# Kernel optimization log

Hardware: AMD Instinct MI355X
Metric: run time of the kernel (lower is better)

Reference implementation:

```python
import jax, jax.numpy as jnp
import numpy as np

B = 131072      # batch
G = 8           # number of groups
GS = 8          # features per group (n_features = G*GS = 64)
K = 8           # n_basis
O = 16          # kan_out_dim
TOT = G * O     # 128, GroupKANLayer output dim
R = 10          # n_rules
FIN = 20        # fuzzy_in_dim = max(2*n_rules, 8)
EPS_BN = 1e-5


def setup_inputs() -> dict:
    key = jax.random.key(0)
    ks = jax.random.split(key, 8)
    x = jax.random.normal(ks[0], (B, G * GS), dtype=jnp.float32)
    # per-group GaussianRBF params (one shared RBF per group, applied to each feature)
    rbf_centres = jnp.tile(jnp.linspace(-3.0, 3.0, K, dtype=jnp.float32)[None, :], (G, 1))
    rbf_log_widths = jnp.zeros((G, K), dtype=jnp.float32)
    rbf_weights = jax.random.normal(ks[1], (G, K), dtype=jnp.float32) * 0.1
    rbf_linear_w = jnp.ones((G,), dtype=jnp.float32)
    # group projections: kaiming normal fan_in (relu gain sqrt(2))
    proj_W = jax.random.normal(ks[2], (G, O, GS), dtype=jnp.float32) * np.sqrt(2.0 / GS)
    proj_b = jnp.zeros((G, O), dtype=jnp.float32)
    bn1_gamma = jnp.ones((TOT,), dtype=jnp.float32)
    bn1_beta = jnp.zeros((TOT,), dtype=jnp.float32)
    # fuzzy_proj linear (xavier uniform) TOT -> FIN
    a = np.sqrt(6.0 / (TOT + FIN))
    fp_W = jax.random.uniform(ks[3], (FIN, TOT), dtype=jnp.float32, minval=-a, maxval=a)
    fp_b = jnp.zeros((FIN,), dtype=jnp.float32)
    bn2_gamma = jnp.ones((FIN,), dtype=jnp.float32)
    bn2_beta = jnp.zeros((FIN,), dtype=jnp.float32)
    # IT2 fuzzy layer params
    fz_centres = jax.random.uniform(ks[4], (R, FIN), dtype=jnp.float32, minval=-1.0, maxval=1.0)
    fz_log_su = jnp.full((R, FIN), -0.7, dtype=jnp.float32)
    fz_log_sl = jnp.full((R, FIN), -1.2, dtype=jnp.float32)
    # sparse rule head
    head_W = jax.random.normal(ks[5], (1, R), dtype=jnp.float32) * 0.05
    head_b = jnp.zeros((1,), dtype=jnp.float32)
    return {
        'x': x, 'rbf_centres': rbf_centres, 'rbf_log_widths': rbf_log_widths,
        'rbf_weights': rbf_weights, 'rbf_linear_w': rbf_linear_w,
        'proj_W': proj_W, 'proj_b': proj_b,
        'bn1_gamma': bn1_gamma, 'bn1_beta': bn1_beta,
        'fp_W': fp_W, 'fp_b': fp_b, 'bn2_gamma': bn2_gamma, 'bn2_beta': bn2_beta,
        'fz_centres': fz_centres, 'fz_log_su': fz_log_su, 'fz_log_sl': fz_log_sl,
        'head_W': head_W, 'head_b': head_b,
    }


def _batchnorm(h, gamma, beta):
    # training-mode BatchNorm1d: normalize with batch mean / biased variance
    mu = h.mean(axis=0)
    var = h.var(axis=0)
    return (h - mu) * jax.lax.rsqrt(var + EPS_BN) * gamma + beta


def _forward(x, rbf_centres, rbf_log_widths, rbf_weights, rbf_linear_w,
             proj_W, proj_b, bn1_gamma, bn1_beta, fp_W, fp_b,
             bn2_gamma, bn2_beta, fz_centres, fz_log_su, fz_log_sl,
             head_W, head_b):
    b = x.shape[0]
    xg = x.reshape(b, G, GS)                               # groups are contiguous index slices
    sigma = jnp.exp(rbf_log_widths) + 1e-6                 # [G,K]
    # Gaussian RBF over all groups/features at once: [B,G,GS,K]
    rbf = jnp.exp(-0.5 * ((xg[..., None] - rbf_centres[:, None, :]) / sigma[:, None, :]) ** 2)
    act = rbf_linear_w[None, :, None] * xg + jnp.einsum('bgfk,gk->bgf', rbf, rbf_weights)
    proj = jnp.einsum('bgf,gof->bgo', act, proj_W) + proj_b  # grouped linear, [B,G,O]
    h = _batchnorm(proj.reshape(b, TOT), bn1_gamma, bn1_beta)
    # fuzzy_proj: Linear -> BN -> GELU (torch default GELU = exact erf form)
    z = _batchnorm(h @ fp_W.T + fp_b, bn2_gamma, bn2_beta)
    z = jax.nn.gelu(z, approximate=False)                    # [B,FIN]
    # IT2 fuzzy memberships
    su = jnp.exp(fz_log_su) + 1e-6                           # [R,FIN]
    sl = jnp.minimum(jnp.exp(fz_log_sl) + 1e-6, su * 0.9)
    diff = z[:, None, :] - fz_centres[None]                  # [B,R,FIN]
    upper = jnp.exp(-0.5 * (diff / su[None]) ** 2).mean(-1)  # [B,R]
    lower = jnp.exp(-0.5 * (diff / sl[None]) ** 2).mean(-1)
    firing = 0.5 * (upper + lower)
    return firing @ head_W.T + head_b                        # [B,1]


def reference(x, rbf_centres, rbf_log_widths, rbf_weights, rbf_linear_w,
              proj_W, proj_b, bn1_gamma, bn1_beta, fp_W, fp_b,
              bn2_gamma, bn2_beta, fz_centres, fz_log_su, fz_log_sl,
              head_W, head_b):
    return _forward(x, rbf_centres, rbf_log_widths, rbf_weights, rbf_linear_w,
                    proj_W, proj_b, bn1_gamma, bn1_beta, fp_W, fp_b,
                    bn2_gamma, bn2_beta, fz_centres, fz_log_su, fz_log_sl,
                    head_W, head_b)
```

## Files before the change

### kernel.cpp

```cpp
#include <hip/hip_runtime.h>
#include <hip/hip_fp16.h>
#include <math.h>

#define B_N 131072

#define WS_STAT1 0
#define ST1_SZ   (64 * 352)
#define WS_MT    22528
#define WS_C     23808
#define WS_STAT2 23840
#define WS_NH    26400
#define WS_ACTH  26816
#define WS_Z     (26816 + (size_t)B_N * 32)
#define WS_END   (WS_Z + (size_t)B_N * 20)

struct alignas(16) H8 { __half2 a, b, c, d; };

__device__ __forceinline__ float gelu_exact(float v) {
    return 0.5f * v * (1.0f + erff(v * 0.70710678118654752440f));
}

__global__ __launch_bounds__(256) void k_act_moments(
    const float* __restrict__ x, const float* __restrict__ cen,
    const float* __restrict__ lw, const float* __restrict__ rw,
    const float* __restrict__ linw, __half* __restrict__ act_h,
    float* __restrict__ stat1, int store)
{
    __shared__ float sAcc[4][8][44];
    const int t = threadIdx.x;
    const int g = t & 7;
    const int rl = t >> 3;

    float c_[8], nh_[8], w_[8];
#pragma unroll
    for (int k = 0; k < 8; ++k) {
        c_[k] = cen[g * 8 + k];
        float s = expf(lw[g * 8 + k]) + 1e-6f;
        nh_[k] = -0.5f / (s * s);
        w_[k] = rw[g * 8 + k];
    }
    const float lin = linw[g];
    const float c0 = c_[0], nh0 = nh_[0];
    const float delta = c_[1] - c_[0];

    bool uni = true;
#pragma unroll
    for (int k = 0; k < 8; ++k) {
        float ck = c0 + (float)k * delta;
        uni = uni && (fabsf(c_[k] - ck) <= 1e-5f * (1.0f + fabsf(ck)));
        uni = uni && (fabsf(nh_[k] - nh0) <= 1e-6f * fabsf(nh0));
    }
    const bool fast = (bool)__all((int)uni);

    float W_[8];
    float k1 = 0.0f;
    if (fast) {
        k1 = -2.0f * delta * nh0;
#pragma unroll
        for (int k = 0; k < 8; ++k) {
            float kd = (float)k * delta;
            W_[k] = w_[k] * __expf(nh0 * kd * kd);
        }
    }

    float sumA[8], P[36];
#pragma unroll
    for (int f = 0; f < 8; ++f) sumA[f] = 0.0f;
#pragma unroll
    for (int i = 0; i < 36; ++i) P[i] = 0.0f;

    if (fast) {
#pragma unroll 1
        for (int row = blockIdx.x * 32 + rl; row < B_N; row += gridDim.x * 32) {
            const float* xr = x + (size_t)row * 64 + g * 8;
            float4 v0 = *(const float4*)(xr);
            float4 v1 = *(const float4*)(xr + 4);
            float xv[8] = {v0.x, v0.y, v0.z, v0.w, v1.x, v1.y, v1.z, v1.w};
            float act[8];
#pragma unroll
            for (int f = 0; f < 8; ++f) {
                float v = xv[f];
                float dv = v - c0;
                float E0 = __expf(nh0 * dv * dv);
                float T  = __expf(k1 * dv);
                float poly = W_[7];
#pragma unroll
                for (int k = 6; k >= 0; --k) poly = poly * T + W_[k];
                act[f] = lin * v + E0 * poly;
            }
            if (store) {
                H8 h;
                h.a = __floats2half2_rn(act[0], act[1]);
                h.b = __floats2half2_rn(act[2], act[3]);
                h.c = __floats2half2_rn(act[4], act[5]);
                h.d = __floats2half2_rn(act[6], act[7]);
                *(H8*)(act_h + (size_t)row * 64 + g * 8) = h;
            }
            int idx = 0;
#pragma unroll
            for (int f = 0; f < 8; ++f) {
                sumA[f] += act[f];
#pragma unroll
                for (int f2 = 0; f2 <= f; ++f2) { P[idx] += act[f] * act[f2]; ++idx; }
            }
        }
    } else {
#pragma unroll 1
        for (int row = blockIdx.x * 32 + rl; row < B_N; row += gridDim.x * 32) {
            const float* xr = x + (size_t)row * 64 + g * 8;
            float4 v0 = *(const float4*)(xr);
            float4 v1 = *(const float4*)(xr + 4);
            float xv[8] = {v0.x, v0.y, v0.z, v0.w, v1.x, v1.y, v1.z, v1.w};
            float act[8];
#pragma unroll
            for (int f = 0; f < 8; ++f) {
                float v = xv[f];
                float a = lin * v;
#pragma unroll
                for (int k = 0; k < 8; ++k) {
                    float d = v - c_[k];
                    a += w_[k] * __expf(d * d * nh_[k]);
                }
                act[f] = a;
            }
            if (store) {
                H8 h;
                h.a = __floats2half2_rn(act[0], act[1]);
                h.b = __floats2half2_rn(act[2], act[3]);
                h.c = __floats2half2_rn(act[4], act[5]);
                h.d = __floats2half2_rn(act[6], act[7]);
                *(H8*)(act_h + (size_t)row * 64 + g * 8) = h;
            }
            int idx = 0;
#pragma unroll
            for (int f = 0; f < 8; ++f) {
                sumA[f] += act[f];
#pragma unroll
                for (int f2 = 0; f2 <= f; ++f2) { P[idx] += act[f] * act[f2]; ++idx; }
            }
        }
    }

#pragma unroll
    for (int off = 32; off >= 8; off >>= 1) {
#pragma unroll
        for (int f = 0; f < 8; ++f) sumA[f] += __shfl_down(sumA[f], off, 64);
#pragma unroll
        for (int i = 0; i < 36; ++i) P[i] += __shfl_down(P[i], off, 64);
    }
    const int wave = t >> 6, lane = t & 63;
    if (lane < 8) {
        float* dst = &sAcc[wave][lane][0];
#pragma unroll
        for (int f = 0; f < 8; ++f) dst[f] = sumA[f];
#pragma unroll
        for (int i = 0; i < 36; ++i) dst[8 + i] = P[i];
    }
    __syncthreads();
    for (int i = t; i < 352; i += 256) {
        int gg = i / 44, v = i % 44;
        float s = sAcc[0][gg][v] + sAcc[1][gg][v] + sAcc[2][gg][v] + sAcc[3][gg][v];
        atomicAdd(&stat1[(blockIdx.x & 63) * 352 + i], s);
    }
}

__global__ __launch_bounds__(256) void k_build(
    const float* __restrict__ stat1, const float* __restrict__ fpW,
    const float* __restrict__ fpb, const float* __restrict__ g1,
    const float* __restrict__ b1, const float* __restrict__ Wp,
    const float* __restrict__ pb, const float* __restrict__ lsu,
    const float* __restrict__ lsl,
    float* __restrict__ Mt, float* __restrict__ Cc, float* __restrict__ nh,
    float* __restrict__ stat2)
{
    __shared__ float Am[8][8];
    __shared__ float Sg[8][36];
    __shared__ float a_[128], bb_[128];
    const int t = threadIdx.x;
    for (int i = t; i < 352; i += 256) {
        float s = 0.0f;
        for (int st = 0; st < 64; ++st) s += stat1[st * 352 + i];
        float m = s * (1.0f / B_N);
        int g = i / 44, v = i % 44;
        if (v < 8) Am[g][v] = m; else Sg[g][v - 8] = m;
    }
    __syncthreads();
    if (t < 128) {
        const int g = t >> 4;
        float wv[8];
#pragma unroll
        for (int f = 0; f < 8; ++f) wv[f] = Wp[t * 8 + f];
        float dot = 0.0f;
#pragma unroll
        for (int f = 0; f < 8; ++f) dot += wv[f] * Am[g][f];
        const float pbv = pb[t];
        const float mu = pbv + dot;
        float e2 = pbv * pbv + 2.0f * pbv * dot;
        int idx = 0;
#pragma unroll
        for (int f = 0; f < 8; ++f)
#pragma unroll
            for (int f2 = 0; f2 <= f; ++f2) {
                float c2 = (f2 == f) ? 1.0f : 2.0f;
                e2 += c2 * wv[f] * wv[f2] * Sg[g][idx]; ++idx;
            }
        const float var = fmaxf(e2 - mu * mu, 0.0f);
        const float a = g1[t] * rsqrtf(var + 1e-5f);
        a_[t] = a;
        bb_[t] = b1[t] - mu * a;
    }
    __syncthreads();
    for (int i = t; i < 1280; i += 256) {
        int gf = i / 20, j = i % 20;
        int g = gf >> 3, f = gf & 7;
        float m = 0.0f;
        for (int o = 0; o < 16; ++o) {
            int c = g * 16 + o;
            m += fpW[j * 128 + c] * a_[c] * Wp[c * 8 + f];
        }
        Mt[i] = m;
    }
    if (t < 20) {
        float cj = fpb[t];
        for (int c = 0; c < 128; ++c)
            cj += fpW[t * 128 + c] * (a_[c] * pb[c] + bb_[c]);
        Cc[t] = cj;
    }
    for (int i = t; i < 200; i += 256) {
        float su = expf(lsu[i]) + 1e-6f;
        float sl = fminf(expf(lsl[i]) + 1e-6f, 0.9f * su);
        nh[i] = -0.5f / (su * su);
        nh[200 + i] = -0.5f / (sl * sl);
    }
    for (int i = t; i < 2560; i += 256) stat2[i] = 0.0f;
}

__global__ __launch_bounds__(256) void k_z(
    const __half* __restrict__ act_h, const float* __restrict__ Mt,
    const float* __restrict__ Cc, float* __restrict__ zout,
    float* __restrict__ stat2)
{
    __shared__ float sRed[4][40];
    const int t = threadIdx.x;
    const int row = blockIdx.x * 256 + t;

    float zp[20];
#pragma unroll
    for (int j = 0; j < 20; ++j) zp[j] = Cc[j];

#pragma unroll 1
    for (int g = 0; g < 8; ++g) {
        const H8 h = *(const H8*)(act_h + (size_t)row * 64 + g * 8);
        float2 f0 = __half22float2(h.a), f1 = __half22float2(h.b);
        float2 f2 = __half22float2(h.c), f3 = __half22float2(h.d);
        float a[8] = {f0.x, f0.y, f1.x, f1.y, f2.x, f2.y, f3.x, f3.y};
#pragma unroll
        for (int f = 0; f < 8; ++f) {
            const float* m = Mt + (g * 8 + f) * 20;
            float av = a[f];
#pragma unroll
            for (int j = 0; j < 20; ++j) zp[j] += av * m[j];
        }
    }

#pragma unroll
    for (int j = 0; j < 20; ++j) zout[(size_t)j * B_N + row] = zp[j];

    float s_[20], q_[20];
#pragma unroll
    for (int j = 0; j < 20; ++j) { s_[j] = zp[j]; q_[j] = zp[j] * zp[j]; }
#pragma unroll
    for (int off = 32; off >= 1; off >>= 1) {
#pragma unroll
        for (int j = 0; j < 20; ++j) {
            s_[j] += __shfl_down(s_[j], off, 64);
            q_[j] += __shfl_down(q_[j], off, 64);
        }
    }
    const int wave = t >> 6, lane = t & 63;
    if (lane == 0) {
#pragma unroll
        for (int j = 0; j < 20; ++j) { sRed[wave][j] = s_[j]; sRed[wave][20 + j] = q_[j]; }
    }
    __syncthreads();
    if (t < 40) {
        float v = sRed[0][t] + sRed[1][t] + sRed[2][t] + sRed[3][t];
        atomicAdd(&stat2[(blockIdx.x & 63) * 40 + t], v);
    }
}

__global__ __launch_bounds__(256) void k_zpre_stats(
    const float* __restrict__ x, const float* __restrict__ cen,
    const float* __restrict__ lw, const float* __restrict__ rw,
    const float* __restrict__ linw, const float* __restrict__ Mt,
    const float* __restrict__ Cc, float* __restrict__ zout,
    float* __restrict__ stat2)
{
    __shared__ __align__(16) float4 sRbf[64];
    __shared__ float sLin[8], sC[20];
    __shared__ __align__(16) float sMt[1280];
    __shared__ float sRed[4][40];
    const int t = threadIdx.x;
    if (t < 64) {
        float s = expf(lw[t]) + 1e-6f;
        sRbf[t] = make_float4(cen[t], rw[t], -0.5f / (s * s), 0.0f);
    }
    if (t < 8)  sLin[t] = linw[t];
    if (t < 20) sC[t] = Cc[t];
    for (int i = t; i < 1280; i += 256) sMt[i] = Mt[i];
    __syncthreads();
    const int row = blockIdx.x * 256 + t;
    const float* xr = x + (size_t)row * 64;
    float zp[20];
#pragma unroll
    for (int j = 0; j < 20; ++j) zp[j] = sC[j];
#pragma unroll 1
    for (int g = 0; g < 8; ++g) {
        float4 v0 = *(const float4*)(xr + g * 8);
        float4 v1 = *(const float4*)(xr + g * 8 + 4);
        float xv[8] = {v0.x, v0.y, v0.z, v0.w, v1.x, v1.y, v1.z, v1.w};
        float act[8];
        float lin = sLin[g];
#pragma unroll
        for (int f = 0; f < 8; ++f) act[f] = lin * xv[f];
#pragma unroll 1
        for (int k = 0; k < 8; ++k) {
            float4 p = sRbf[g * 8 + k];
#pragma unroll
            for (int f = 0; f < 8; ++f) {
                float d = xv[f] - p.x;
                act[f] += p.y * __expf(d * d * p.z);
            }
        }
#pragma unroll 1
        for (int f = 0; f < 8; ++f) {
            float av = act[f];
            const float4* m4 = (const float4*)(sMt + (g * 8 + f) * 20);
            float4 ma = m4[0], mb = m4[1], mc = m4[2], md = m4[3], me = m4[4];
            zp[0] += av * ma.x; zp[1] += av * ma.y; zp[2] += av * ma.z; zp[3] += av * ma.w;
            zp[4] += av * mb.x; zp[5] += av * mb.y; zp[6] += av * mb.z; zp[7] += av * mb.w;
            zp[8] += av * mc.x; zp[9] += av * mc.y; zp[10] += av * mc.z; zp[11] += av * mc.w;
            zp[12] += av * md.x; zp[13] += av * md.y; zp[14] += av * md.z; zp[15] += av * md.w;
            zp[16] += av * me.x; zp[17] += av * me.y; zp[18] += av * me.z; zp[19] += av * me.w;
        }
    }
#pragma unroll
    for (int j = 0; j < 20; ++j) zout[(size_t)j * B_N + row] = zp[j];
    float s_[20], q_[20];
#pragma unroll
    for (int j = 0; j < 20; ++j) { s_[j] = zp[j]; q_[j] = zp[j] * zp[j]; }
#pragma unroll
    for (int off = 32; off >= 1; off >>= 1) {
#pragma unroll
        for (int j = 0; j < 20; ++j) {
            s_[j] += __shfl_down(s_[j], off, 64);
            q_[j] += __shfl_down(q_[j], off, 64);
        }
    }
    const int wave = t >> 6, lane = t & 63;
    if (lane == 0) {
#pragma unroll
        for (int j = 0; j < 20; ++j) { sRed[wave][j] = s_[j]; sRed[wave][20 + j] = q_[j]; }
    }
    __syncthreads();
    if (t < 40) {
        float v = sRed[0][t] + sRed[1][t] + sRed[2][t] + sRed[3][t];
        atomicAdd(&stat2[(blockIdx.x & 63) * 40 + t], v);
    }
}

__global__ __launch_bounds__(256) void k_out(
    const float* __restrict__ zin, const float* __restrict__ stat2,
    const float* __restrict__ g2, const float* __restrict__ b2,
    const float* __restrict__ nh, const float* __restrict__ fzc,
    const float* __restrict__ hW, const float* __restrict__ hb,
    float* __restrict__ out)
{
    __shared__ float sT[40], sSc[20], sSh[20];
    const int t = threadIdx.x;
    if (t < 40) {
        float s = 0.0f;
        for (int st = 0; st < 64; ++st) s += stat2[st * 40 + t];
        sT[t] = s;
    }
    __syncthreads();
    if (t < 20) {
        float mu = sT[t] * (1.0f / B_N);
        float var = fmaxf(sT[20 + t] * (1.0f / B_N) - mu * mu, 0.0f);
        float sc = g2[t] * rsqrtf(var + 1e-5f);
        sSc[t] = sc;
        sSh[t] = b2[t] - mu * sc;
    }
    __syncthreads();

    const int row = blockIdx.x * 256 + t;
    float z[20];
#pragma unroll
    for (int j = 0; j < 20; ++j) {
        float v = zin[(size_t)j * B_N + row];
        z[j] = gelu_exact(sSc[j] * v + sSh[j]);
    }
    float acc = hb[0];
#pragma unroll 1
    for (int r = 0; r < 10; ++r) {
        float u = 0.0f, l = 0.0f;
#pragma unroll
        for (int j = 0; j < 20; ++j) {
            float cx = fzc[r * 20 + j];
            float pu = nh[r * 20 + j];
            float pl = nh[200 + r * 20 + j];
            float d = z[j] - cx;
            float dd = d * d;
            u += __expf(dd * pu);
            l += __expf(dd * pl);
        }
        acc += hW[r] * 0.025f * (u + l);
    }
    out[row] = acc;
}

extern "C" void kernel_launch(void* const* d_in, const int* in_sizes, int n_in,
                              void* d_out, int out_size, void* d_ws, size_t ws_size,
                              hipStream_t stream) {
    const float* x    = (const float*)d_in[0];
    const float* cen  = (const float*)d_in[1];
    const float* lw   = (const float*)d_in[2];
    const float* rw   = (const float*)d_in[3];
    const float* linw = (const float*)d_in[4];
    const float* Wp   = (const float*)d_in[5];
    const float* pb   = (const float*)d_in[6];
    const float* g1   = (const float*)d_in[7];
    const float* b1   = (const float*)d_in[8];
    const float* fpW  = (const float*)d_in[9];
    const float* fpb  = (const float*)d_in[10];
    const float* g2   = (const float*)d_in[11];
    const float* b2   = (const float*)d_in[12];
    const float* fzc  = (const float*)d_in[13];
    const float* lsu  = (const float*)d_in[14];
    const float* lsl  = (const float*)d_in[15];
    const float* hW   = (const float*)d_in[16];
    const float* hb   = (const float*)d_in[17];

    float* ws    = (float*)d_ws;
    float* stat1 = ws + WS_STAT1;
    float* Mt    = ws + WS_MT;
    float* Cc    = ws + WS_C;
    float* stat2 = ws + WS_STAT2;
    float* nh    = ws + WS_NH;
    __half* acth = (__half*)(ws + WS_ACTH);
    float* zbuf  = ws + WS_Z;
    float* outp  = (float*)d_out;

    const size_t needFull = WS_END * sizeof(float);
    const int mode = (ws_size >= needFull) ? 2 : 1;
    if (mode == 1) zbuf = ws + WS_ACTH;

    hipMemsetAsync(stat1, 0, (size_t)ST1_SZ * sizeof(float), stream);
    k_act_moments<<<1024, 256, 0, stream>>>(x, cen, lw, rw, linw, acth, stat1,
                                            mode == 2 ? 1 : 0);
    k_build<<<1, 256, 0, stream>>>(stat1, fpW, fpb, g1, b1, Wp, pb, lsu, lsl,
                                   Mt, Cc, nh, stat2);
    if (mode == 2) {
        k_z<<<512, 256, 0, stream>>>(acth, Mt, Cc, zbuf, stat2);
    } else {
        k_zpre_stats<<<512, 256, 0, stream>>>(x, cen, lw, rw, linw, Mt, Cc,
                                              zbuf, stat2);
    }
    k_out<<<512, 256, 0, stream>>>(zbuf, stat2, g2, b2, nh, fzc, hW, hb, outp);
}
```

Before: 166.2 us.

## Recompute RBF activations in z pass instead of storing fp16 intermediates

Drops the fp16 activation buffer written by the moments pass and read back by the z pass. The z pass now reloads x and recomputes the RBF activations, using a fast factored-exponential path when centres are uniformly spaced with equal widths. The build kernel precomputes the RBF coefficients and a uniformity flag. This trades roughly 16 MB of write plus 16 MB of read traffic for extra transcendental math and a second 32 MB read of x, and it also removes the fp16 rounding of activations.

```diff
diff --git a/kernel.cpp b/kernel.cpp
--- a/kernel.cpp
+++ b/kernel.cpp
@@ -1,5 +1,4 @@
 #include <hip/hip_runtime.h>
-#include <hip/hip_fp16.h>
 #include <math.h>
 
 #define B_N 131072
@@ -10,11 +9,10 @@
 #define WS_C     23808
 #define WS_STAT2 23840
 #define WS_NH    26400
-#define WS_ACTH  26816
-#define WS_Z     (26816 + (size_t)B_N * 32)
+#define WS_RBFF  26816
+#define WS_RBFX  26944
+#define WS_Z     28672
 #define WS_END   (WS_Z + (size_t)B_N * 20)
-
-struct alignas(16) H8 { __half2 a, b, c, d; };
 
 __device__ __forceinline__ float gelu_exact(float v) {
     return 0.5f * v * (1.0f + erff(v * 0.70710678118654752440f));
@@ -23,8 +21,7 @@
 __global__ __launch_bounds__(256) void k_act_moments(
     const float* __restrict__ x, const float* __restrict__ cen,
     const float* __restrict__ lw, const float* __restrict__ rw,
-    const float* __restrict__ linw, __half* __restrict__ act_h,
-    float* __restrict__ stat1, int store)
+    const float* __restrict__ linw, float* __restrict__ stat1)
 {
     __shared__ float sAcc[4][8][44];
     const int t = threadIdx.x;
@@ -88,14 +85,6 @@
                 for (int k = 6; k >= 0; --k) poly = poly * T + W_[k];
                 act[f] = lin * v + E0 * poly;
             }
-            if (store) {
-                H8 h;
-                h.a = __floats2half2_rn(act[0], act[1]);
-                h.b = __floats2half2_rn(act[2], act[3]);
-                h.c = __floats2half2_rn(act[4], act[5]);
-                h.d = __floats2half2_rn(act[6], act[7]);
-                *(H8*)(act_h + (size_t)row * 64 + g * 8) = h;
-            }
             int idx = 0;
 #pragma unroll
             for (int f = 0; f < 8; ++f) {
@@ -123,14 +112,6 @@
                 }
                 act[f] = a;
             }
-            if (store) {
-                H8 h;
-                h.a = __floats2half2_rn(act[0], act[1]);
-                h.b = __floats2half2_rn(act[2], act[3]);
-                h.c = __floats2half2_rn(act[4], act[5]);
-                h.d = __floats2half2_rn(act[6], act[7]);
-                *(H8*)(act_h + (size_t)row * 64 + g * 8) = h;
-            }
             int idx = 0;
 #pragma unroll
             for (int f = 0; f < 8; ++f) {
@@ -169,9 +150,11 @@
     const float* __restrict__ fpb, const float* __restrict__ g1,
     const float* __restrict__ b1, const float* __restrict__ Wp,
     const float* __restrict__ pb, const float* __restrict__ lsu,
-    const float* __restrict__ lsl,
+    const float* __restrict__ lsl, const float* __restrict__ cen,
+    const float* __restrict__ lw, const float* __restrict__ rw,
+    const float* __restrict__ linw,
     float* __restrict__ Mt, float* __restrict__ Cc, float* __restrict__ nh,
-    float* __restrict__ stat2)
+    float* __restrict__ stat2, float* __restrict__ rbff, float* __restrict__ rbfx)
 {
     __shared__ float Am[8][8];
     __shared__ float Sg[8][36];
@@ -233,119 +216,132 @@
         nh[200 + i] = -0.5f / (sl * sl);
     }
     for (int i = t; i < 2560; i += 256) stat2[i] = 0.0f;
+
+    if (t < 64) {
+        float s = expf(lw[t]) + 1e-6f;
+        rbfx[t]        = cen[t];
+        rbfx[64 + t]   = rw[t];
+        rbfx[128 + t]  = -0.5f / (s * s);
+    }
+    if (t < 8) {
+        const int g = t;
+        float c0 = cen[g * 8];
+        float delta = cen[g * 8 + 1] - c0;
+        float s0 = expf(lw[g * 8]) + 1e-6f;
+        float nh0 = -0.5f / (s0 * s0);
+        rbff[8 + g * 4 + 0] = c0;
+        rbff[8 + g * 4 + 1] = -2.0f * delta * nh0;
+        rbff[8 + g * 4 + 2] = nh0;
+        rbff[8 + g * 4 + 3] = linw[g];
+    }
+    if (t >= 64 && t < 128) {
+        const int i = t - 64;
+        const int g = i >> 3, k = i & 7;
+        float delta = cen[g * 8 + 1] - cen[g * 8];
+        float s0 = expf(lw[g * 8]) + 1e-6f;
+        float nh0 = -0.5f / (s0 * s0);
+        float kd = (float)k * delta;
+        rbff[64 + i] = rw[i] * __expf(nh0 * kd * kd);
+    }
+    if (t == 0) {
+        bool uni = true;
+        for (int g = 0; g < 8; ++g) {
+            float c0 = cen[g * 8];
+            float delta = cen[g * 8 + 1] - c0;
+            float s0 = expf(lw[g * 8]) + 1e-6f;
+            float nh0 = -0.5f / (s0 * s0);
+            for (int k = 0; k < 8; ++k) {
+                float ck = c0 + (float)k * delta;
+                uni = uni && (fabsf(cen[g * 8 + k] - ck) <= 1e-5f * (1.0f + fabsf(ck)));
+                float sk = expf(lw[g * 8 + k]) + 1e-6f;
+                float nhk = -0.5f / (sk * sk);
+                uni = uni && (fabsf(nhk - nh0) <= 1e-6f * fabsf(nh0));
+            }
+        }
+        rbff[0] = uni ? 1.0f : 0.0f;
+    }
 }
 
 __global__ __launch_bounds__(256) void k_z(
-    const __half* __restrict__ act_h, const float* __restrict__ Mt,
-    const float* __restrict__ Cc, float* __restrict__ zout,
-    float* __restrict__ stat2)
+    const float* __restrict__ x, const float* __restrict__ Mt,
+    const float* __restrict__ Cc, const float* __restrict__ rbff,
+    const float* __restrict__ rbfx, const float* __restrict__ linw,
+    float* __restrict__ zout, float* __restrict__ stat2)
 {
     __shared__ float sRed[4][40];
     const int t = threadIdx.x;
     const int row = blockIdx.x * 256 + t;
+    const float* xr = x + (size_t)row * 64;
 
     float zp[20];
 #pragma unroll
     for (int j = 0; j < 20; ++j) zp[j] = Cc[j];
 
-#pragma unroll 1
-    for (int g = 0; g < 8; ++g) {
-        const H8 h = *(const H8*)(act_h + (size_t)row * 64 + g * 8);
-        float2 f0 = __half22float2(h.a), f1 = __half22float2(h.b);
-        float2 f2 = __half22float2(h.c), f3 = __half22float2(h.d);
-        float a[8] = {f0.x, f0.y, f1.x, f1.y, f2.x, f2.y, f3.x, f3.y};
-#pragma unroll
-        for (int f = 0; f < 8; ++f) {
-            const float* m = Mt + (g * 8 + f) * 20;
-            float av = a[f];
-#pragma unroll
-            for (int j = 0; j < 20; ++j) zp[j] += av * m[j];
+    const bool fast = rbff[0] > 0.5f;
+    if (fast) {
+#pragma unroll 1
+        for (int g = 0; g < 8; ++g) {
+            const float c0  = rbff[8 + g * 4 + 0];
+            const float k1  = rbff[8 + g * 4 + 1];
+            const float nh0 = rbff[8 + g * 4 + 2];
+            const float lin = rbff[8 + g * 4 + 3];
+            float4 v0 = *(const float4*)(xr + g * 8);
+            float4 v1 = *(const float4*)(xr + g * 8 + 4);
+            float xv[8] = {v0.x, v0.y, v0.z, v0.w, v1.x, v1.y, v1.z, v1.w};
+            float act[8];
+#pragma unroll
+            for (int f = 0; f < 8; ++f) {
+                float v = xv[f];
+                float dv = v - c0;
+                float E0 = __expf(nh0 * dv * dv);
+                float T  = __expf(k1 * dv);
+                float poly = rbff[64 + g * 8 + 7];
+#pragma unroll
+                for (int k = 6; k >= 0; --k) poly = poly * T + rbff[64 + g * 8 + k];
+                act[f] = lin * v + E0 * poly;
+            }
+#pragma unroll
+            for (int f = 0; f < 8; ++f) {
+                const float* m = Mt + (g * 8 + f) * 20;
+                float av = act[f];
+#pragma unroll
+                for (int j = 0; j < 20; ++j) zp[j] += av * m[j];
+            }
+        }
+    } else {
+#pragma unroll 1
+        for (int g = 0; g < 8; ++g) {
+            const float lin = linw[g];
+            float4 v0 = *(const float4*)(xr + g * 8);
+            float4 v1 = *(const float4*)(xr + g * 8 + 4);
+            float xv[8] = {v0.x, v0.y, v0.z, v0.w, v1.x, v1.y, v1.z, v1.w};
+            float act[8];
+#pragma unroll
+            for (int f = 0; f < 8; ++f) act[f] = lin * xv[f];
+#pragma unroll 1
+            for (int k = 0; k < 8; ++k) {
+                const float ck = rbfx[g * 8 + k];
+                const float wk = rbfx[64 + g * 8 + k];
+                const float nk = rbfx[128 + g * 8 + k];
+#pragma unroll
+                for (int f = 0; f < 8; ++f) {
+                    float d = xv[f] - ck;
+                    act[f] += wk * __expf(d * d * nk);
+                }
+            }
+#pragma unroll
+            for (int f = 0; f < 8; ++f) {
+                const float* m = Mt + (g * 8 + f) * 20;
+                float av = act[f];
+#pragma unroll
+                for (int j = 0; j < 20; ++j) zp[j] += av * m[j];
+            }
         }
     }
 
 #pragma unroll
     for (int j = 0; j < 20; ++j) zout[(size_t)j * B_N + row] = zp[j];
 
-    float s_[20], q_[20];
-#pragma unroll
-    for (int j = 0; j < 20; ++j) { s_[j] = zp[j]; q_[j] = zp[j] * zp[j]; }
-#pragma unroll
-    for (int off = 32; off >= 1; off >>= 1) {
-#pragma unroll
-        for (int j = 0; j < 20; ++j) {
-            s_[j] += __shfl_down(s_[j], off, 64);
-            q_[j] += __shfl_down(q_[j], off, 64);
-        }
-    }
-    const int wave = t >> 6, lane = t & 63;
-    if (lane == 0) {
-#pragma unroll
-        for (int j = 0; j < 20; ++j) { sRed[wave][j] = s_[j]; sRed[wave][20 + j] = q_[j]; }
-    }
-    __syncthreads();
-    if (t < 40) {
-        float v = sRed[0][t] + sRed[1][t] + sRed[2][t] + sRed[3][t];
-        atomicAdd(&stat2[(blockIdx.x & 63) * 40 + t], v);
-    }
-}
-
-__global__ __launch_bounds__(256) void k_zpre_stats(
-    const float* __restrict__ x, const float* __restrict__ cen,
-    const float* __restrict__ lw, const float* __restrict__ rw,
-    const float* __restrict__ linw, const float* __restrict__ Mt,
-    const float* __restrict__ Cc, float* __restrict__ zout,
-    float* __restrict__ stat2)
-{
-    __shared__ __align__(16) float4 sRbf[64];
-    __shared__ float sLin[8], sC[20];
-    __shared__ __align__(16) float sMt[1280];
-    __shared__ float sRed[4][40];
-    const int t = threadIdx.x;
-    if (t < 64) {
-        float s = expf(lw[t]) + 1e-6f;
-        sRbf[t] = make_float4(cen[t], rw[t], -0.5f / (s * s), 0.0f);
-    }
-    if (t < 8)  sLin[t] = linw[t];
-    if (t < 20) sC[t] = Cc[t];
-    for (int i = t; i < 1280; i += 256) sMt[i] = Mt[i];
-    __syncthreads();
-    const int row = blockIdx.x * 256 + t;
-    const float* xr = x + (size_t)row * 64;
-    float zp[20];
-#pragma unroll
-    for (int j = 0; j < 20; ++j) zp[j] = sC[j];
-#pragma unroll 1
-    for (int g = 0; g < 8; ++g) {
-        float4 v0 = *(const float4*)(xr + g * 8);
-        float4 v1 = *(const float4*)(xr + g * 8 + 4);
-        float xv[8] = {v0.x, v0.y, v0.z, v0.w, v1.x, v1.y, v1.z, v1.w};
-        float act[8];
-        float lin = sLin[g];
-#pragma unroll
-        for (int f = 0; f < 8; ++f) act[f] = lin * xv[f];
-#pragma unroll 1
-        for (int k = 0; k < 8; ++k) {
-            float4 p = sRbf[g * 8 + k];
-#pragma unroll
-            for (int f = 0; f < 8; ++f) {
-                float d = xv[f] - p.x;
-                act[f] += p.y * __expf(d * d * p.z);
-            }
-        }
-#pragma unroll 1
-        for (int f = 0; f < 8; ++f) {
-            float av = act[f];
-            const float4* m4 = (const float4*)(sMt + (g * 8 + f) * 20);
-            float4 ma = m4[0], mb = m4[1], mc = m4[2], md = m4[3], me = m4[4];
-            zp[0] += av * ma.x; zp[1] += av * ma.y; zp[2] += av * ma.z; zp[3] += av * ma.w;
-            zp[4] += av * mb.x; zp[5] += av * mb.y; zp[6] += av * mb.z; zp[7] += av * mb.w;
-            zp[8] += av * mc.x; zp[9] += av * mc.y; zp[10] += av * mc.z; zp[11] += av * mc.w;
-            zp[12] += av * md.x; zp[13] += av * md.y; zp[14] += av * md.z; zp[15] += av * md.w;
-            zp[16] += av * me.x; zp[17] += av * me.y; zp[18] += av * me.z; zp[19] += av * me.w;
-        }
-    }
-#pragma unroll
-    for (int j = 0; j < 20; ++j) zout[(size_t)j * B_N + row] = zp[j];
     float s_[20], q_[20];
 #pragma unroll
     for (int j = 0; j < 20; ++j) { s_[j] = zp[j]; q_[j] = zp[j] * zp[j]; }
@@ -447,24 +443,16 @@
     float* Cc    = ws + WS_C;
     float* stat2 = ws + WS_STAT2;
     float* nh    = ws + WS_NH;
-    __half* acth = (__half*)(ws + WS_ACTH);
+    float* rbff  = ws + WS_RBFF;
+    float* rbfx  = ws + WS_RBFX;
     float* zbuf  = ws + WS_Z;
     float* outp  = (float*)d_out;
 
-    const size_t needFull = WS_END * sizeof(float);
-    const int mode = (ws_size >= needFull) ? 2 : 1;
-    if (mode == 1) zbuf = ws + WS_ACTH;
-
     hipMemsetAsync(stat1, 0, (size_t)ST1_SZ * sizeof(float), stream);
-    k_act_moments<<<1024, 256, 0, stream>>>(x, cen, lw, rw, linw, acth, stat1,
-                                            mode == 2 ? 1 : 0);
+    k_act_moments<<<1024, 256, 0, stream>>>(x, cen, lw, rw, linw, stat1);
     k_build<<<1, 256, 0, stream>>>(stat1, fpW, fpb, g1, b1, Wp, pb, lsu, lsl,
-                                   Mt, Cc, nh, stat2);
-    if (mode == 2) {
-        k_z<<<512, 256, 0, stream>>>(acth, Mt, Cc, zbuf, stat2);
-    } else {
-        k_zpre_stats<<<512, 256, 0, stream>>>(x, cen, lw, rw, linw, Mt, Cc,
-                                              zbuf, stat2);
-    }
+                                   cen, lw, rw, linw,
+                                   Mt, Cc, nh, stat2, rbff, rbfx);
+    k_z<<<512, 256, 0, stream>>>(x, Mt, Cc, rbff, rbfx, linw, zbuf, stat2);
     k_out<<<512, 256, 0, stream>>>(zbuf, stat2, g2, b2, nh, fzc, hW, hb, outp);
 }
```

Measured after the change: 177.7 us. 1.07x slower.
